# Optimization experiments

Measured on AMD Instinct MI355X. Metric: run time of the kernel, lower is better.

Reference implementation:

```python
import jax, jax.numpy as jnp
import numpy as np

B, S, D_MODEL = 2, 2048, 2048
N_HEADS, N_KV = 16, 4
HEAD_DIM = D_MODEL // N_HEADS  # 128
N_REP = N_HEADS // N_KV        # 4


def _apply_rope(x, cos, sin):
    # x: [B, H, S, Dh]; cos/sin: [S, Dh//2]
    c = cos[None, None, :, :]
    s = sin[None, None, :, :]
    x_even = x[..., ::2]
    x_odd = x[..., 1::2]
    re = x_even * c - x_odd * s
    ro = x_even * s + x_odd * c
    # interleave back: stack on last axis then flatten -> [..., Dh]
    return jnp.stack([re, ro], axis=-1).reshape(x.shape)


def setup_inputs() -> dict:
    key = jax.random.key(0)
    ks = jax.random.split(key, 7)
    std = 1.0 / np.sqrt(D_MODEL)
    return {
        "x": jax.random.normal(ks[0], (B, S, D_MODEL), dtype=jnp.float32),
        "rope_cos": jax.random.uniform(ks[1], (S, HEAD_DIM // 2), dtype=jnp.float32),
        "rope_sin": jax.random.uniform(ks[2], (S, HEAD_DIM // 2), dtype=jnp.float32),
        "Wq": jax.random.normal(ks[3], (D_MODEL, N_HEADS * HEAD_DIM), dtype=jnp.float32) * std,
        "Wk": jax.random.normal(ks[4], (D_MODEL, N_KV * HEAD_DIM), dtype=jnp.float32) * std,
        "Wv": jax.random.normal(ks[5], (D_MODEL, N_KV * HEAD_DIM), dtype=jnp.float32) * std,
        "Wo": jax.random.normal(ks[6], (N_HEADS * HEAD_DIM, D_MODEL), dtype=jnp.float32) * std,
    }


def reference(x, rope_cos, rope_sin, Wq, Wk, Wv, Wo):
    batch, seq_len, _ = x.shape
    q = (x @ Wq).reshape(batch, seq_len, N_HEADS, HEAD_DIM).transpose(0, 2, 1, 3)
    k = (x @ Wk).reshape(batch, seq_len, N_KV, HEAD_DIM).transpose(0, 2, 1, 3)
    v = (x @ Wv).reshape(batch, seq_len, N_KV, HEAD_DIM).transpose(0, 2, 1, 3)

    q = _apply_rope(q, rope_cos[:seq_len], rope_sin[:seq_len])
    k = _apply_rope(k, rope_cos[:seq_len], rope_sin[:seq_len])

    # GQA: group q heads by kv head instead of materializing repeated k/v.
    qg = q.reshape(batch, N_KV, N_REP, seq_len, HEAD_DIM)
    scale = 1.0 / np.sqrt(HEAD_DIM)
    scores = jnp.einsum('bgrqd,bgkd->bgrqk', qg, k) * scale

    causal = jnp.tril(jnp.ones((seq_len, seq_len), dtype=bool))
    scores = jnp.where(causal[None, None, None, :, :], scores, -jnp.inf)
    weights = jax.nn.softmax(scores, axis=-1)

    out = jnp.einsum('bgrqk,bgkd->bgrqd', weights, v)
    out = out.reshape(batch, N_HEADS, seq_len, HEAD_DIM).transpose(0, 2, 1, 3)
    out = out.reshape(batch, seq_len, N_HEADS * HEAD_DIM)
    return out @ Wo
```

## Files before the change

kernel.cpp:

```cpp
#include <hip/hip_runtime.h>
#include <hip/hip_bf16.h>
#include <math.h>

typedef __bf16 bf16x8_t __attribute__((ext_vector_type(8)));
typedef float f32x4 __attribute__((ext_vector_type(4)));
typedef unsigned short ushort8 __attribute__((ext_vector_type(8)));

__device__ inline unsigned short f2bf(float f) {
  unsigned int u = __builtin_bit_cast(unsigned int, f);
  u += 0x7fffu + ((u >> 16) & 1u);
  return (unsigned short)(u >> 16);
}
__device__ inline float b2f(unsigned short s) {
  unsigned int u = ((unsigned int)s) << 16;
  return __builtin_bit_cast(float, u);
}
__device__ inline unsigned int pack2bf(float lo, float hi) {
  return (unsigned int)f2bf(lo) | ((unsigned int)f2bf(hi) << 16);
}

__device__ __forceinline__ void gll16(const void* g, void* l) {
  __builtin_amdgcn_global_load_lds((const __attribute__((address_space(1))) void*)g,
                                   (__attribute__((address_space(3))) void*)l, 16, 0, 0);
}

__global__ void cvt_k(const float* __restrict__ X, unsigned short* __restrict__ Xb, int total8) {
  int i = blockIdx.x * blockDim.x + threadIdx.x;
  if (i >= total8) return;
  const float4* p = (const float4*)X + 2 * (size_t)i;
  float4 a = p[0], b = p[1];
  ushort8 v;
  v[0] = f2bf(a.x); v[1] = f2bf(a.y); v[2] = f2bf(a.z); v[3] = f2bf(a.w);
  v[4] = f2bf(b.x); v[5] = f2bf(b.y); v[6] = f2bf(b.z); v[7] = f2bf(b.w);
  ((ushort8*)Xb)[i] = v;
}

__global__ void twc_k(const float* __restrict__ W, unsigned short* __restrict__ Wt, int K, int N) {
  __shared__ float tile[32][33];
  int k0 = blockIdx.x * 32, n0 = blockIdx.y * 32;
  int tx = threadIdx.x, ty = threadIdx.y;
#pragma unroll
  for (int i = 0; i < 32; i += 8) tile[ty + i][tx] = W[(size_t)(k0 + ty + i) * N + n0 + tx];
  __syncthreads();
#pragma unroll
  for (int i = 0; i < 32; i += 8)
    Wt[(size_t)(n0 + ty + i) * K + k0 + tx] = f2bf(tile[tx][ty + i]);
}

template <bool OUT_BF16, bool ROPE>
__global__ __launch_bounds__(256) void gemm_tn(const unsigned short* __restrict__ A,
                                               const unsigned short* __restrict__ Bt,
                                               void* __restrict__ Cv, int M, int N, int K,
                                               const float* __restrict__ cs,
                                               const float* __restrict__ sn, int ropeLim) {
  __shared__ __align__(16) unsigned short As[2][128 * 32];
  __shared__ __align__(16) unsigned short Bs[2][128 * 32];
  const int t = threadIdx.x, w = t >> 6, lane = t & 63;
  const int la = lane & 15, lk = lane >> 4;
  const int wr = w >> 1, wc = w & 1;
  const int bm = blockIdx.y * 128, bn = blockIdx.x * 128;
  const int lrow = lane >> 2, lcb = (lane & 3) * 8;

  const unsigned short* Ab = A + (size_t)(bm + (w * 2) * 16 + lrow) * K + lcb;
  const unsigned short* Ab1 = A + (size_t)(bm + (w * 2 + 1) * 16 + lrow) * K + lcb;
  const unsigned short* Bb = Bt + (size_t)(bn + (w * 2) * 16 + lrow) * K + lcb;
  const unsigned short* Bb1 = Bt + (size_t)(bn + (w * 2 + 1) * 16 + lrow) * K + lcb;
  const int c0 = w * 2, c1 = w * 2 + 1;

  f32x4 acc[4][4] = {};

  gll16(Ab, (char*)As[0] + c0 * 1024);
  gll16(Ab1, (char*)As[0] + c1 * 1024);
  gll16(Bb, (char*)Bs[0] + c0 * 1024);
  gll16(Bb1, (char*)Bs[0] + c1 * 1024);

  const int nt = K / 32;
  int cur = 0;
  for (int kt = 0; kt < nt; ++kt) {
    __syncthreads();
    if (kt + 1 < nt) {
      const int kn = (kt + 1) * 32;
      gll16(Ab + kn, (char*)As[cur ^ 1] + c0 * 1024);
      gll16(Ab1 + kn, (char*)As[cur ^ 1] + c1 * 1024);
      gll16(Bb + kn, (char*)Bs[cur ^ 1] + c0 * 1024);
      gll16(Bb1 + kn, (char*)Bs[cur ^ 1] + c1 * 1024);
    }

    bf16x8_t a[4], b[4];
#pragma unroll
    for (int m = 0; m < 4; ++m)
      a[m] = __builtin_bit_cast(
          bf16x8_t, *(const ushort8*)(As[cur] + (wr * 64 + m * 16 + la) * 32 + lk * 8));
#pragma unroll
    for (int n = 0; n < 4; ++n)
      b[n] = __builtin_bit_cast(
          bf16x8_t, *(const ushort8*)(Bs[cur] + (wc * 64 + n * 16 + la) * 32 + lk * 8));
#pragma unroll
    for (int m = 0; m < 4; ++m)
#pragma unroll
      for (int n = 0; n < 4; ++n)
        acc[m][n] = __builtin_amdgcn_mfma_f32_16x16x32_bf16(a[m], b[n], acc[m][n], 0, 0, 0);
    cur ^= 1;
  }

#pragma unroll
  for (int m = 0; m < 4; ++m) {
#pragma unroll
    for (int n = 0; n < 4; ++n) {
      const int col = bn + wc * 64 + n * 16 + la;
      const bool doRope = ROPE && (col < ropeLim);
#pragma unroll
      for (int r = 0; r < 4; ++r) {
        int row = bm + wr * 64 + m * 16 + lk * 4 + r;
        float val = acc[m][n][r];
        if (ROPE) {
          float pval = __shfl_xor(val, 1);
          if (doRope) {
            int srow = row & 2047;
            int i = (col & 127) >> 1;
            float cc = cs[srow * 64 + i], ss = sn[srow * 64 + i];
            val = (la & 1) ? (pval * ss + val * cc) : (val * cc - pval * ss);
          }
        }
        if (OUT_BF16)
          ((unsigned short*)Cv)[(size_t)row * N + col] = f2bf(val);
        else
          ((float*)Cv)[(size_t)row * N + col] = val;
      }
    }
  }
}

__global__ void transpose_v(const unsigned short* __restrict__ QKV, unsigned short* __restrict__ Vt) {
  __shared__ unsigned short tile[32][33];
  int bg = blockIdx.z;
  int b = bg >> 2, g = bg & 3;
  int s0 = blockIdx.x * 32, d0 = blockIdx.y * 32;
  int tx = threadIdx.x, ty = threadIdx.y;
#pragma unroll
  for (int i = 0; i < 32; i += 8)
    tile[ty + i][tx] = QKV[((size_t)(b * 2048 + s0 + ty + i)) * 3072 + 2560 + g * 128 + d0 + tx];
  __syncthreads();
#pragma unroll
  for (int i = 0; i < 32; i += 8)
    Vt[((size_t)(bg * 128 + d0 + ty + i)) * 2048 + s0 + tx] = tile[tx][ty + i];
}

__global__ __launch_bounds__(256, 2) void attn_mfma(const unsigned short* __restrict__ QKV,
                                                    const unsigned short* __restrict__ Vt,
                                                    unsigned short* __restrict__ Ob) {
  const int S = 2048;
  __shared__ __align__(16) unsigned short Ks[2][64 * 128];
  __shared__ __align__(16) unsigned short Vs[2][128 * 64];
  __shared__ __align__(16) unsigned short Ps[4 * 32 * 64];

  const int t = threadIdx.x;
  const int w = t >> 6, lane = t & 63;
  const int la = lane & 15, lk = lane >> 4;
  const int b = blockIdx.z, h = blockIdx.y, g = h >> 2;
  const int qt = (b == 0) ? (gridDim.x - 1 - blockIdx.x) : blockIdx.x;
  const int q0 = qt * 128;
  const int qw = q0 + w * 32;
  const float scale = 0.08838834764831845f;

  const unsigned short* ksrc[4];
  const unsigned short* vsrc[4];
#pragma unroll
  for (int u = 0; u < 4; ++u) {
    int kr = 16 * w + 4 * u + (lane >> 4);
    int kp = lane & 15;
    ksrc[u] = QKV + (size_t)(b * S + kr) * 3072 + 2048 + g * 128 + (kp ^ (kr & 7)) * 8;
    int vr = 32 * w + 8 * u + (lane >> 3);
    int vp = lane & 7;
    vsrc[u] = Vt + (size_t)((b * 4 + g) * 128 + vr) * 2048 + (vp ^ (vr & 7)) * 8;
  }

  bf16x8_t qf[2][4];
#pragma unroll
  for (int qi = 0; qi < 2; ++qi)
#pragma unroll
    for (int dt = 0; dt < 4; ++dt)
      qf[qi][dt] = __builtin_bit_cast(
          bf16x8_t, *(const ushort8*)(QKV + (size_t)(b * S + qw + qi * 16 + la) * 3072 + h * 128 +
                                      dt * 32 + lk * 8));

  f32x4 oa[2][8];
#pragma unroll
  for (int qi = 0; qi < 2; ++qi)
#pragma unroll
    for (int dt = 0; dt < 8; ++dt) oa[qi][dt] = (f32x4){0.f, 0.f, 0.f, 0.f};
  float mr[2] = {-1e30f, -1e30f}, lr[2] = {0.f, 0.f};

  const int n_kt = 2 * qt + 2;
  const int kmask0 = qw & ~63;
  char* pw = (char*)Ps + w * 4096;

#pragma unroll
  for (int u = 0; u < 4; ++u) {
    gll16(ksrc[u], (char*)Ks[0] + (4 * w + u) * 1024);
    gll16(vsrc[u], (char*)Vs[0] + (4 * w + u) * 1024);
  }
  __syncthreads();

  int cur = 0;
  for (int kt = 0; kt < n_kt; ++kt) {
    const int k0 = kt * 64;
    if (kt + 1 < n_kt) {
      const int kn = k0 + 64;
#pragma unroll
      for (int u = 0; u < 4; ++u) {
        gll16(ksrc[u] + (size_t)kn * 3072, (char*)Ks[cur ^ 1] + (4 * w + u) * 1024);
        gll16(vsrc[u] + kn, (char*)Vs[cur ^ 1] + (4 * w + u) * 1024);
      }
    }

    if (k0 <= qw + 31) {
      char* Ksb = (char*)Ks[cur];
      char* Vsb = (char*)Vs[cur];

      f32x4 sacc[2][4];
#pragma unroll
      for (int qi = 0; qi < 2; ++qi)
#pragma unroll
        for (int ktc = 0; ktc < 4; ++ktc) sacc[qi][ktc] = (f32x4){0.f, 0.f, 0.f, 0.f};
      __builtin_amdgcn_s_setprio(1);
#pragma unroll
      for (int ktc = 0; ktc < 4; ++ktc) {
        int row = ktc * 16 + la;
#pragma unroll
        for (int dt = 0; dt < 4; ++dt) {
          bf16x8_t kf = __builtin_bit_cast(
              bf16x8_t, *(const ushort8*)(Ksb + row * 256 + ((((dt << 2) + lk) ^ (row & 7)) << 4)));
          sacc[0][ktc] = __builtin_amdgcn_mfma_f32_16x16x32_bf16(kf, qf[0][dt], sacc[0][ktc], 0, 0, 0);
          sacc[1][ktc] = __builtin_amdgcn_mfma_f32_16x16x32_bf16(kf, qf[1][dt], sacc[1][ktc], 0, 0, 0);
        }
      }
      __builtin_amdgcn_s_setprio(0);

      const bool domask = (k0 == kmask0);
#pragma unroll
      for (int qi = 0; qi < 2; ++qi) {
        const int q = qw + qi * 16 + la;
        float p[4][4];
        float tm = -1e30f;
#pragma unroll
        for (int ktc = 0; ktc < 4; ++ktc)
#pragma unroll
          for (int r = 0; r < 4; ++r) {
            float sv = sacc[qi][ktc][r] * scale;
            if (domask && (k0 + ktc * 16 + lk * 4 + r > q)) sv = -1e30f;
            p[ktc][r] = sv;
            tm = fmaxf(tm, sv);
          }
        tm = fmaxf(tm, __shfl_xor(tm, 16));
        tm = fmaxf(tm, __shfl_xor(tm, 32));
        float mn;
        if (__all(tm - mr[qi] <= 8.f)) {
          mn = mr[qi];
        } else {
          mn = fmaxf(mr[qi], tm);
          float sc = __expf(mr[qi] - mn);
          mr[qi] = mn;
          lr[qi] *= sc;
          float scb[4];
#pragma unroll
          for (int r = 0; r < 4; ++r) scb[r] = __shfl(sc, lk * 4 + r);
#pragma unroll
          for (int dt = 0; dt < 8; ++dt)
#pragma unroll
            for (int r = 0; r < 4; ++r) oa[qi][dt][r] *= scb[r];
        }
        float ts = 0.f;
#pragma unroll
        for (int ktc = 0; ktc < 4; ++ktc)
#pragma unroll
          for (int r = 0; r < 4; ++r) {
            float e = __expf(p[ktc][r] - mn);
            p[ktc][r] = e;
            ts += e;
          }
        ts += __shfl_xor(ts, 16);
        ts += __shfl_xor(ts, 32);
        lr[qi] += ts;
        char* pq = pw + (qi * 16 + la) * 128;
#pragma unroll
        for (int ktc = 0; ktc < 4; ++ktc) {
          uint2 gv;
          gv.x = pack2bf(p[ktc][0], p[ktc][1]);
          gv.y = pack2bf(p[ktc][2], p[ktc][3]);
          *(uint2*)(pq + ((32 * ktc + 8 * lk) ^ ((la & 7) << 4))) = gv;
        }
      }
      asm volatile("s_waitcnt lgkmcnt(0)" ::: "memory");

      bf16x8_t pf[2][2];
#pragma unroll
      for (int qi = 0; qi < 2; ++qi)
#pragma unroll
        for (int ks = 0; ks < 2; ++ks)
          pf[qi][ks] = __builtin_bit_cast(
              bf16x8_t, *(const ushort8*)(pw + (qi * 16 + la) * 128 +
                                          ((64 * ks + 16 * lk) ^ ((la & 7) << 4))));
      __builtin_amdgcn_s_setprio(1);
#pragma unroll
      for (int dt = 0; dt < 8; ++dt) {
        int d = dt * 16 + la;
#pragma unroll
        for (int ks = 0; ks < 2; ++ks) {
          bf16x8_t vf = __builtin_bit_cast(
              bf16x8_t, *(const ushort8*)(Vsb + d * 128 + ((((ks << 2) + lk) ^ (d & 7)) << 4)));
          oa[0][dt] = __builtin_amdgcn_mfma_f32_16x16x32_bf16(pf[0][ks], vf, oa[0][dt], 0, 0, 0);
          oa[1][dt] = __builtin_amdgcn_mfma_f32_16x16x32_bf16(pf[1][ks], vf, oa[1][dt], 0, 0, 0);
        }
      }
      __builtin_amdgcn_s_setprio(0);
    }

    __syncthreads();
    cur ^= 1;
  }

#pragma unroll
  for (int qi = 0; qi < 2; ++qi) {
    float inv = 1.f / lr[qi];
    float invb[4];
#pragma unroll
    for (int r = 0; r < 4; ++r) invb[r] = __shfl(inv, lk * 4 + r);
#pragma unroll
    for (int dt = 0; dt < 8; ++dt)
#pragma unroll
      for (int r = 0; r < 4; ++r)
        Ob[(size_t)(b * S + qw + qi * 16 + lk * 4 + r) * 2048 + h * 128 + dt * 16 + la] =
            f2bf(oa[qi][dt][r] * invb[r]);
  }
}

extern "C" void kernel_launch(void* const* d_in, const int* in_sizes, int n_in,
                              void* d_out, int out_size, void* d_ws, size_t ws_size,
                              hipStream_t stream) {
  const float* x = (const float*)d_in[0];
  const float* rc = (const float*)d_in[1];
  const float* rs = (const float*)d_in[2];
  const float* Wq = (const float*)d_in[3];
  const float* Wk = (const float*)d_in[4];
  const float* Wv = (const float*)d_in[5];
  const float* Wo = (const float*)d_in[6];
  float* out = (float*)d_out;

  const int B = 2, S = 2048, DM = 2048;
  const int M = B * S;

  unsigned short* xb = (unsigned short*)d_ws;
  unsigned short* QKV = xb + (size_t)M * DM;
  unsigned short* WallT = QKV + (size_t)M * 3072;
  unsigned short* WoT = WallT;
  unsigned short* Vt = WallT + (size_t)2048 * 2048;
  unsigned short* Ob = xb;

  dim3 blk(256);

  cvt_k<<<(M * DM / 8 + 255) / 256, blk, 0, stream>>>(x, xb, M * DM / 8);
  twc_k<<<dim3(64, 64), dim3(32, 8), 0, stream>>>(Wq, WallT, DM, DM);
  twc_k<<<dim3(64, 16), dim3(32, 8), 0, stream>>>(Wk, WallT + (size_t)2048 * DM, DM, 512);
  twc_k<<<dim3(64, 16), dim3(32, 8), 0, stream>>>(Wv, WallT + (size_t)2560 * DM, DM, 512);

  gemm_tn<true, true><<<dim3(3072 / 128, M / 128), blk, 0, stream>>>(xb, WallT, QKV, M, 3072, DM,
                                                                     rc, rs, 2560);

  twc_k<<<dim3(64, 64), dim3(32, 8), 0, stream>>>(Wo, WoT, DM, DM);

  transpose_v<<<dim3(S / 32, 4, B * 4), dim3(32, 8), 0, stream>>>(QKV, Vt);

  attn_mfma<<<dim3(S / 128, 16, B), dim3(256), 0, stream>>>(QKV, Vt, Ob);

  gemm_tn<false, false><<<dim3(DM / 128, M / 128), blk, 0, stream>>>(Ob, WoT, out, M, DM, DM,
                                                                     nullptr, nullptr, 0);
}
```

Before: 233.3 us.

## Split long causal query tiles across two KV chunks and merge with combine kernel

Query tiles with more than 16 KV tiles are split into two blocks, each covering up to 16 KV tiles. The partial outputs and their softmax max/sum statistics go to workspace, and a new combine kernel merges them, which evens out the causal work per block. The K/V staging also changes from double-buffered direct global-to-LDS loads to single-buffered register prefetch. That frees shared memory so launch bounds can be raised to 3 blocks per CU, at the cost of an extra sync per tile and an extra kernel launch plus partial-result traffic.

```diff
diff --git a/kernel.cpp b/kernel.cpp
--- a/kernel.cpp
+++ b/kernel.cpp
@@ -146,34 +146,64 @@
     Vt[((size_t)(bg * 128 + d0 + ty + i)) * 2048 + s0 + tx] = tile[tx][ty + i];
 }
 
-__global__ __launch_bounds__(256, 2) void attn_mfma(const unsigned short* __restrict__ QKV,
+__global__ __launch_bounds__(256, 3) void attn_mfma(const unsigned short* __restrict__ QKV,
                                                     const unsigned short* __restrict__ Vt,
-                                                    unsigned short* __restrict__ Ob) {
+                                                    unsigned short* __restrict__ Ob,
+                                                    unsigned short* __restrict__ oP,
+                                                    float* __restrict__ mlP) {
   const int S = 2048;
-  __shared__ __align__(16) unsigned short Ks[2][64 * 128];
-  __shared__ __align__(16) unsigned short Vs[2][128 * 64];
+  __shared__ __align__(16) unsigned short Ks[64 * 128];
+  __shared__ __align__(16) unsigned short Vs[128 * 64];
   __shared__ __align__(16) unsigned short Ps[4 * 32 * 64];
 
   const int t = threadIdx.x;
   const int w = t >> 6, lane = t & 63;
   const int la = lane & 15, lk = lane >> 4;
   const int b = blockIdx.z, h = blockIdx.y, g = h >> 2;
-  const int qt = (b == 0) ? (gridDim.x - 1 - blockIdx.x) : blockIdx.x;
-  const int q0 = qt * 128;
-  const int qw = q0 + w * 32;
+
+  int x = blockIdx.x, qt, c;
+  if (x < 9) { qt = 7 + x; c = 0; }
+  else if (x == 9) { qt = 15; c = 1; }
+  else { int k = (x - 10) >> 1; if ((x & 1) == 0) { qt = 6 - k; c = 0; } else { qt = 14 - k; c = 1; } }
+
+  const int qw = qt * 128 + w * 32;
+  const int n_full = 2 * qt + 2;
+  const int kts = c * 16;
+  const int kte = min(n_full, kts + 16);
+  const bool full = (kts == 0) && (kte == n_full);
   const float scale = 0.08838834764831845f;
 
-  const unsigned short* ksrc[4];
-  const unsigned short* vsrc[4];
-#pragma unroll
-  for (int u = 0; u < 4; ++u) {
-    int kr = 16 * w + 4 * u + (lane >> 4);
-    int kp = lane & 15;
-    ksrc[u] = QKV + (size_t)(b * S + kr) * 3072 + 2048 + g * 128 + (kp ^ (kr & 7)) * 8;
-    int vr = 32 * w + 8 * u + (lane >> 3);
-    int vp = lane & 7;
-    vsrc[u] = Vt + (size_t)((b * 4 + g) * 128 + vr) * 2048 + (vp ^ (vr & 7)) * 8;
-  }
+  const int skr = t >> 2, skc = t & 3;
+  const int svr = t >> 1, svc = t & 1;
+  const unsigned short* kgp = QKV + (size_t)(b * S + skr) * 3072 + 2048 + g * 128;
+  const unsigned short* vgp = Vt + (size_t)((b * 4 + g) * 128 + svr) * 2048;
+  char* Ksb = (char*)Ks;
+  char* Vsb = (char*)Vs;
+
+  float4 kr0, kr1, kr2, kr3, vr0, vr1, vr2, vr3;
+#define LOADR(KT)                                                          \
+  do {                                                                     \
+    const size_t _ko = (size_t)(KT) * 64;                                  \
+    kr0 = *(const float4*)(kgp + _ko * 3072 + (skc + 0) * 8);              \
+    kr1 = *(const float4*)(kgp + _ko * 3072 + (skc + 4) * 8);              \
+    kr2 = *(const float4*)(kgp + _ko * 3072 + (skc + 8) * 8);              \
+    kr3 = *(const float4*)(kgp + _ko * 3072 + (skc + 12) * 8);             \
+    vr0 = *(const float4*)(vgp + _ko + (svc + 0) * 8);                     \
+    vr1 = *(const float4*)(vgp + _ko + (svc + 2) * 8);                     \
+    vr2 = *(const float4*)(vgp + _ko + (svc + 4) * 8);                     \
+    vr3 = *(const float4*)(vgp + _ko + (svc + 6) * 8);                     \
+  } while (0)
+#define WRITEL()                                                             \
+  do {                                                                       \
+    *(float4*)(Ksb + skr * 256 + (((skc + 0) ^ (skr & 7)) << 4)) = kr0;      \
+    *(float4*)(Ksb + skr * 256 + (((skc + 4) ^ (skr & 7)) << 4)) = kr1;      \
+    *(float4*)(Ksb + skr * 256 + (((skc + 8) ^ (skr & 7)) << 4)) = kr2;      \
+    *(float4*)(Ksb + skr * 256 + (((skc + 12) ^ (skr & 7)) << 4)) = kr3;     \
+    *(float4*)(Vsb + svr * 128 + (((svc + 0) ^ (svr & 7)) << 4)) = vr0;      \
+    *(float4*)(Vsb + svr * 128 + (((svc + 2) ^ (svr & 7)) << 4)) = vr1;      \
+    *(float4*)(Vsb + svr * 128 + (((svc + 4) ^ (svr & 7)) << 4)) = vr2;      \
+    *(float4*)(Vsb + svr * 128 + (((svc + 6) ^ (svr & 7)) << 4)) = vr3;      \
+  } while (0)
 
   bf16x8_t qf[2][4];
 #pragma unroll
@@ -191,33 +221,18 @@
     for (int dt = 0; dt < 8; ++dt) oa[qi][dt] = (f32x4){0.f, 0.f, 0.f, 0.f};
   float mr[2] = {-1e30f, -1e30f}, lr[2] = {0.f, 0.f};
 
-  const int n_kt = 2 * qt + 2;
   const int kmask0 = qw & ~63;
   char* pw = (char*)Ps + w * 4096;
 
-#pragma unroll
-  for (int u = 0; u < 4; ++u) {
-    gll16(ksrc[u], (char*)Ks[0] + (4 * w + u) * 1024);
-    gll16(vsrc[u], (char*)Vs[0] + (4 * w + u) * 1024);
-  }
+  LOADR(kts);
+  WRITEL();
   __syncthreads();
 
-  int cur = 0;
-  for (int kt = 0; kt < n_kt; ++kt) {
+  for (int kt = kts; kt < kte; ++kt) {
     const int k0 = kt * 64;
-    if (kt + 1 < n_kt) {
-      const int kn = k0 + 64;
-#pragma unroll
-      for (int u = 0; u < 4; ++u) {
-        gll16(ksrc[u] + (size_t)kn * 3072, (char*)Ks[cur ^ 1] + (4 * w + u) * 1024);
-        gll16(vsrc[u] + kn, (char*)Vs[cur ^ 1] + (4 * w + u) * 1024);
-      }
-    }
+    if (kt + 1 < kte) LOADR(kt + 1);
 
     if (k0 <= qw + 31) {
-      char* Ksb = (char*)Ks[cur];
-      char* Vsb = (char*)Vs[cur];
-
       f32x4 sacc[2][4];
 #pragma unroll
       for (int qi = 0; qi < 2; ++qi)
@@ -317,21 +332,78 @@
     }
 
     __syncthreads();
-    cur ^= 1;
+    if (kt + 1 < kte) {
+      WRITEL();
+      __syncthreads();
+    }
   }
 
-#pragma unroll
-  for (int qi = 0; qi < 2; ++qi) {
-    float inv = 1.f / lr[qi];
-    float invb[4];
-#pragma unroll
-    for (int r = 0; r < 4; ++r) invb[r] = __shfl(inv, lk * 4 + r);
-#pragma unroll
-    for (int dt = 0; dt < 8; ++dt)
-#pragma unroll
-      for (int r = 0; r < 4; ++r)
-        Ob[(size_t)(b * S + qw + qi * 16 + lk * 4 + r) * 2048 + h * 128 + dt * 16 + la] =
-            f2bf(oa[qi][dt][r] * invb[r]);
+  if (full) {
+#pragma unroll
+    for (int qi = 0; qi < 2; ++qi) {
+      float inv = 1.f / lr[qi];
+      float invb[4];
+#pragma unroll
+      for (int r = 0; r < 4; ++r) invb[r] = __shfl(inv, lk * 4 + r);
+#pragma unroll
+      for (int dt = 0; dt < 8; ++dt)
+#pragma unroll
+        for (int r = 0; r < 4; ++r)
+          Ob[(size_t)(b * S + qw + qi * 16 + lk * 4 + r) * 2048 + h * 128 + dt * 16 + la] =
+              f2bf(oa[qi][dt][r] * invb[r]);
+    }
+  } else {
+    const int slot = (b * 16 + h) * 8 + (qt - 8);
+    unsigned short* op = oP + ((size_t)slot * 2 + c) * (128 * 128);
+    float* ml = mlP + ((size_t)slot * 2 + c) * 256;
+#pragma unroll
+    for (int qi = 0; qi < 2; ++qi) {
+      if (lk == 0) {
+        ml[w * 32 + qi * 16 + la] = mr[qi];
+        ml[128 + w * 32 + qi * 16 + la] = lr[qi];
+      }
+      float inv = 1.f / lr[qi];
+      float invb[4];
+#pragma unroll
+      for (int r = 0; r < 4; ++r) invb[r] = __shfl(inv, lk * 4 + r);
+#pragma unroll
+      for (int dt = 0; dt < 8; ++dt)
+#pragma unroll
+        for (int r = 0; r < 4; ++r)
+          op[(size_t)(w * 32 + qi * 16 + lk * 4 + r) * 128 + dt * 16 + la] =
+              f2bf(oa[qi][dt][r] * invb[r]);
+    }
+  }
+#undef LOADR
+#undef WRITEL
+}
+
+__global__ __launch_bounds__(256) void combine_k(const unsigned short* __restrict__ oP,
+                                                 const float* __restrict__ mlP,
+                                                 unsigned short* __restrict__ Ob) {
+  const int slot = blockIdx.x;
+  const int b = slot >> 7, h = (slot >> 3) & 15, qt = 8 + (slot & 7);
+  const int t = threadIdx.x;
+  const int r = t >> 1, half = t & 1;
+  const float* ml0 = mlP + (size_t)slot * 512;
+  const float* ml1 = ml0 + 256;
+  float m0 = ml0[r], l0 = ml0[128 + r], m1 = ml1[r], l1 = ml1[128 + r];
+  float M = fmaxf(m0, m1);
+  float w0 = l0 * __expf(m0 - M), w1 = l1 * __expf(m1 - M);
+  float inv = 1.f / (w0 + w1);
+  w0 *= inv;
+  w1 *= inv;
+  const unsigned short* o0 = oP + (size_t)slot * 2 * 16384 + r * 128 + half * 64;
+  const unsigned short* o1 = o0 + 16384;
+  unsigned short* ob = Ob + (size_t)(b * 2048 + qt * 128 + r) * 2048 + h * 128 + half * 64;
+#pragma unroll
+  for (int j = 0; j < 64; j += 8) {
+    ushort8 a = *(const ushort8*)(o0 + j);
+    ushort8 c = *(const ushort8*)(o1 + j);
+    ushort8 o;
+#pragma unroll
+    for (int e = 0; e < 8; ++e) o[e] = f2bf(w0 * b2f(a[e]) + w1 * b2f(c[e]));
+    *(ushort8*)(ob + j) = o;
   }
 }
 
@@ -356,6 +428,8 @@
   unsigned short* WoT = WallT;
   unsigned short* Vt = WallT + (size_t)2048 * 2048;
   unsigned short* Ob = xb;
+  unsigned short* oP = WallT + (size_t)3072 * 2048;
+  float* mlP = (float*)(oP + (size_t)256 * 2 * 16384);
 
   dim3 blk(256);
 
@@ -371,7 +445,8 @@
 
   transpose_v<<<dim3(S / 32, 4, B * 4), dim3(32, 8), 0, stream>>>(QKV, Vt);
 
-  attn_mfma<<<dim3(S / 128, 16, B), dim3(256), 0, stream>>>(QKV, Vt, Ob);
+  attn_mfma<<<dim3(24, 16, B), blk, 0, stream>>>(QKV, Vt, Ob, oP, mlP);
+  combine_k<<<dim3(256), blk, 0, stream>>>(oP, mlP, Ob);
 
   gemm_tn<false, false><<<dim3(DM / 128, M / 128), blk, 0, stream>>>(Ob, WoT, out, M, DM, DM,
                                                                      nullptr, nullptr, 0);
```

New measurement: 368.2 us. 57.8% more time.
